# Kernel tuning notes

Hardware: AMD Instinct MI355X
Metric: run time of the kernel (lower is better)

The kernel has to match this reference:

```python
import jax, jax.numpy as jnp
import numpy as np

B, S, D = 2, 2048, 1024
H, HD = 16, 64
FFN_DIM = 4096
EPS = 1e-10


def layer_norm(x, gamma, beta):
    mean = jnp.mean(x, axis=-1, keepdims=True)
    var = jnp.mean((x - mean) ** 2, axis=-1, keepdims=True)
    return (x - mean) / jnp.sqrt(var + EPS) * gamma + beta


def setup_inputs() -> dict:
    key = jax.random.key(0)
    ks = jax.random.split(key, 12)
    s = lambda fan_in, fan_out: (6.0 / (fan_in + fan_out)) ** 0.5
    u = lambda k, shape, c: jax.random.uniform(k, shape, jnp.float32, -c, c)
    return {
        "x": jax.random.normal(ks[0], (B, S, D), jnp.float32),
        "wq": u(ks[1], (H, D, HD), s(D, HD)),
        "bq": jnp.zeros((H, HD), jnp.float32),
        "wk": u(ks[2], (H, D, HD), s(D, HD)),
        "bk": jnp.zeros((H, HD), jnp.float32),
        "wv": u(ks[3], (H, D, HD), s(D, HD)),
        "bv": jnp.zeros((H, HD), jnp.float32),
        "w_proj": u(ks[4], (D, D), s(D, D)),
        "b_proj": jnp.zeros((D,), jnp.float32),
        "gamma1": jnp.ones((D,), jnp.float32),
        "beta1": jnp.zeros((D,), jnp.float32),
        "w1": u(ks[5], (D, FFN_DIM), (1.0 / D) ** 0.5),
        "b1": jnp.zeros((FFN_DIM,), jnp.float32),
        "w2": u(ks[6], (FFN_DIM, D), (1.0 / FFN_DIM) ** 0.5),
        "b2": jnp.zeros((D,), jnp.float32),
        "gamma2": jnp.ones((D,), jnp.float32),
        "beta2": jnp.zeros((D,), jnp.float32),
    }


def reference(x, wq, bq, wk, bk, wv, bv, w_proj, b_proj, gamma1, beta1,
              w1, b1, w2, b2, gamma2, beta2):
    # multi-head self-attention (all heads batched along axis h)
    q = jnp.einsum("bsd,hde->bhse", x, wq) + bq[None, :, None, :]
    k = jnp.einsum("bsd,hde->bhse", x, wk) + bk[None, :, None, :]
    v = jnp.einsum("bsd,hde->bhse", x, wv) + bv[None, :, None, :]
    # scale by sqrt of per-head dim (emb_dim of projected queries)
    scores = jnp.einsum("bhse,bhte->bhst", q, k) / (HD ** 0.5)
    attn = jax.nn.softmax(scores, axis=-1)
    out_h = jnp.einsum("bhst,bhte->bhse", attn, v)  # [B,H,S,HD]
    concat = out_h.transpose(0, 2, 1, 3).reshape(B, S, D)
    attn_out = concat @ w_proj + b_proj
    # residual + norm1 (dropout=0)
    out1 = layer_norm(attn_out + x, gamma1, beta1)
    # FFN: linear - relu - linear
    ffn_out = jax.nn.relu(out1 @ w1 + b1) @ w2 + b2
    # residual + norm2
    return layer_norm(ffn_out + out1, gamma2, beta2)
```

## Files before the change

kernel.cpp:

```cpp
#include <hip/hip_runtime.h>
#include <stdint.h>

typedef float f32x4 __attribute__((ext_vector_type(4)));
typedef __bf16 bf16x8 __attribute__((ext_vector_type(8)));
typedef __bf16 bf16x8_a __attribute__((ext_vector_type(8), may_alias));
typedef __bf16 bf16x4_a __attribute__((ext_vector_type(4), may_alias));
typedef unsigned int u32x4_a __attribute__((ext_vector_type(4), may_alias));
typedef unsigned short u16x4_a __attribute__((ext_vector_type(4), may_alias));

#define DEV __device__ __forceinline__
#define MFMA_B16(a, b, c) __builtin_amdgcn_mfma_f32_16x16x32_bf16((a), (b), (c), 0, 0, 0)

#if __has_builtin(__builtin_amdgcn_exp2f)
#define EXP2(x) __builtin_amdgcn_exp2f(x)
#else
#define EXP2(x) exp2f(x)
#endif

DEV unsigned short f2b(float f) {
  unsigned int u = __float_as_uint(f);
  u = u + 0x7FFFu + ((u >> 16) & 1u);
  return (unsigned short)(u >> 16);
}
DEV float b2f(unsigned short u) { return __uint_as_float(((unsigned int)u) << 16); }

#define GLOAD_LDS16(gsrc, ldst)                                                  \
  __builtin_amdgcn_global_load_lds(                                              \
      (__attribute__((address_space(1))) void*)(uintptr_t)(const void*)(gsrc),   \
      (__attribute__((address_space(3))) void*)(ldst), 16, 0, 0)

__global__ __launch_bounds__(256) void prepass_kernel(
    const float* __restrict__ x, const float* __restrict__ wq,
    const float* __restrict__ wk, const float* __restrict__ wv,
    const float* __restrict__ w_proj, const float* __restrict__ w1,
    const float* __restrict__ w2, const float* __restrict__ bq,
    const float* __restrict__ bk, const float* __restrict__ bv,
    unsigned short* __restrict__ xb, unsigned short* __restrict__ Wqkv_t,
    unsigned short* __restrict__ o_proj, unsigned short* __restrict__ o1,
    unsigned short* __restrict__ o2, float* __restrict__ biasq) {
  __shared__ float tile[32][33];
  int bid = blockIdx.x;
  if (bid < 4096) {
    int i = bid * 256 + threadIdx.x;
    float4 v = ((const float4*)x)[i];
    u16x4_a t = {f2b(v.x), f2b(v.y), f2b(v.z), f2b(v.w)};
    ((u16x4_a*)xb)[i] = t;
    return;
  }
  bid -= 4096;
  if (bid < 3072) {
    const int bx = bid & 1, by = (bid >> 1) & 31, zz = bid >> 6;
    const int sel = zz >> 4, zh = zz & 15;
    const float scale = sel == 0 ? 0.18033688f : 1.f;
    const float* ip = (sel == 0 ? wq : (sel == 1 ? wk : wv)) + (size_t)zh * 1024 * 64;
    unsigned short* op = Wqkv_t + (size_t)sel * 1024 * 1024 + (size_t)zh * 1024 * 64;
    const int tx = threadIdx.x & 31, ty = threadIdx.x >> 5;
    const int c0 = bx * 32, r0 = by * 32;
#pragma unroll
    for (int j = 0; j < 32; j += 8)
      tile[ty + j][tx] = ip[(size_t)(r0 + ty + j) * 64 + (c0 + tx)];
    __syncthreads();
#pragma unroll
    for (int j = 0; j < 32; j += 8)
      op[(size_t)(c0 + ty + j) * 1024 + (r0 + tx)] = f2b(tile[tx][ty + j] * scale);
    return;
  }
  bid -= 3072;
  if (bid < 9216) {
    const float* in;
    unsigned short* out;
    int rows, cols, bx, by;
    if (bid < 1024) {
      in = w_proj; out = o_proj; rows = 1024; cols = 1024; bx = bid & 31; by = bid >> 5;
    } else if (bid < 5120) {
      bid -= 1024; in = w1; out = o1; rows = 1024; cols = 4096; bx = bid & 127; by = bid >> 7;
    } else {
      bid -= 5120; in = w2; out = o2; rows = 4096; cols = 1024; bx = bid & 31; by = bid >> 5;
    }
    const int tx = threadIdx.x & 31, ty = threadIdx.x >> 5;
    const int c0 = bx * 32, r0 = by * 32;
#pragma unroll
    for (int j = 0; j < 32; j += 8)
      tile[ty + j][tx] = in[(size_t)(r0 + ty + j) * cols + (c0 + tx)];
    __syncthreads();
#pragma unroll
    for (int j = 0; j < 32; j += 8)
      out[(size_t)(c0 + ty + j) * rows + (r0 + tx)] = f2b(tile[tx][ty + j]);
    return;
  }
  bid -= 9216;
  int c = bid * 256 + threadIdx.x;
  int which = c >> 10, idx = c & 1023;
  float v = which == 0 ? bq[idx] : (which == 1 ? bk[idx] : bv[idx]);
  biasq[c] = which == 0 ? v * 0.18033688f : v;
}

template <int EP>
__global__ __launch_bounds__(512, 2) void gemm256_kernel(
    const unsigned short* __restrict__ A, const unsigned short* __restrict__ Bt,
    int M, int N, int K, int nbx, int KS,
    const float* __restrict__ bias, unsigned short* __restrict__ outb,
    unsigned short* __restrict__ q_out, unsigned short* __restrict__ k_out,
    unsigned short* __restrict__ v_out,
    unsigned short* __restrict__ pp0, unsigned short* __restrict__ pp1,
    unsigned short* __restrict__ pp2, unsigned short* __restrict__ pp3) {
  __shared__ __align__(16) unsigned short sA[2][256 * 64];
  __shared__ __align__(16) unsigned short sB[2][256 * 64];

  const int tid = threadIdx.x;
  const int wid = tid >> 6, lane = tid & 63;
  const int g = lane >> 4, r15 = lane & 15;
  const int wm = wid >> 2, wn = wid & 3;

  const int nwg = gridDim.x, cpx = nwg >> 3, orig = blockIdx.x;
  const int wg = (orig & 7) * cpx + (orig >> 3);
  const int bx = wg % nbx;
  const int t1 = wg / nbx;
  const int kz = t1 % KS, by = t1 / KS;
  const int row0 = by * 256, col0 = bx * 256;

  const int tilesK = K >> 6;
  const int qT = tilesK / KS, rT = tilesK % KS;
  const int tile0 = kz * qT + (kz < rT ? kz : rT);
  const int NT = qT + (kz < rT ? 1 : 0);
  const int kbase = tile0 << 6;

  const unsigned short* gA0 = A + (size_t)row0 * K + kbase;
  const unsigned short* gB0 = Bt + (size_t)col0 * K + kbase;
  const int srow8 = lane >> 3;
  const int schunk = ((lane & 7) ^ srow8) * 8;

  f32x4 acc[8][4] = {};
  bf16x8 af[4][2], bfr[4][2];

  auto stA = [&](int buf, int k0, int i) {
    const int r = wid * 32 + i * 8;
    GLOAD_LDS16(gA0 + (size_t)(r + srow8) * K + k0 + schunk, &sA[buf][r * 64]);
  };
  auto stB = [&](int buf, int k0, int i) {
    const int r = wid * 32 + i * 8;
    GLOAD_LDS16(gB0 + (size_t)(r + srow8) * K + k0 + schunk, &sB[buf][r * 64]);
  };
  auto ldA = [&](const unsigned short* p, int m, int ks) -> bf16x8 {
    const int row = wm * 128 + m * 16 + r15;
    return *(const bf16x8_a*)&p[row * 64 + (((ks * 4 + g) ^ (r15 & 7)) * 8)];
  };
  auto ldB = [&](const unsigned short* p, int n, int ks) -> bf16x8 {
    const int row = wn * 64 + n * 16 + r15;
    return *(const bf16x8_a*)&p[row * 64 + (((ks * 4 + g) ^ (r15 & 7)) * 8)];
  };

#pragma unroll
  for (int i = 0; i < 4; ++i) { stA(0, 0, i); stB(0, 0, i); }
  asm volatile("s_waitcnt vmcnt(0)" ::: "memory");
  __builtin_amdgcn_s_barrier();

  for (int kt = 0; kt < NT; ++kt) {
    const int cb = kt & 1, nb = cb ^ 1;
    const bool pf = (kt + 1) < NT;
    const int k1 = (kt + 1) << 6;
    const unsigned short* pA = sA[cb];
    const unsigned short* pB = sB[cb];

#pragma unroll
    for (int m = 0; m < 4; ++m) { af[m][0] = ldA(pA, m, 0); af[m][1] = ldA(pA, m, 1); }
#pragma unroll
    for (int n = 0; n < 4; ++n) { bfr[n][0] = ldB(pB, n, 0); bfr[n][1] = ldB(pB, n, 1); }
    if (pf) { stA(nb, k1, 0); stA(nb, k1, 1); }
    __builtin_amdgcn_s_barrier();
    asm volatile("s_waitcnt lgkmcnt(0)" ::: "memory");
    __builtin_amdgcn_sched_barrier(0);
    __builtin_amdgcn_s_setprio(1);
#pragma unroll
    for (int m = 0; m < 4; ++m)
#pragma unroll
      for (int n = 0; n < 2; ++n) {
        acc[m][n] = MFMA_B16(af[m][0], bfr[n][0], acc[m][n]);
        acc[m][n] = MFMA_B16(af[m][1], bfr[n][1], acc[m][n]);
      }
    __builtin_amdgcn_s_setprio(0);
    __builtin_amdgcn_s_barrier();

    if (pf) { stA(nb, k1, 2); stA(nb, k1, 3); }
    __builtin_amdgcn_s_barrier();
    __builtin_amdgcn_s_setprio(1);
#pragma unroll
    for (int m = 0; m < 4; ++m)
#pragma unroll
      for (int n = 2; n < 4; ++n) {
        acc[m][n] = MFMA_B16(af[m][0], bfr[n][0], acc[m][n]);
        acc[m][n] = MFMA_B16(af[m][1], bfr[n][1], acc[m][n]);
      }
    __builtin_amdgcn_s_setprio(0);
    __builtin_amdgcn_s_barrier();

#pragma unroll
    for (int m = 0; m < 4; ++m) { af[m][0] = ldA(pA, m + 4, 0); af[m][1] = ldA(pA, m + 4, 1); }
    if (pf) { stB(nb, k1, 0); stB(nb, k1, 1); }
    __builtin_amdgcn_s_barrier();
    asm volatile("s_waitcnt lgkmcnt(0)" ::: "memory");
    __builtin_amdgcn_sched_barrier(0);
    __builtin_amdgcn_s_setprio(1);
#pragma unroll
    for (int m = 0; m < 4; ++m)
#pragma unroll
      for (int n = 0; n < 2; ++n) {
        acc[m + 4][n] = MFMA_B16(af[m][0], bfr[n][0], acc[m + 4][n]);
        acc[m + 4][n] = MFMA_B16(af[m][1], bfr[n][1], acc[m + 4][n]);
      }
    __builtin_amdgcn_s_setprio(0);
    __builtin_amdgcn_s_barrier();

    if (pf) { stB(nb, k1, 2); stB(nb, k1, 3); }
    __builtin_amdgcn_s_barrier();
    __builtin_amdgcn_s_setprio(1);
#pragma unroll
    for (int m = 0; m < 4; ++m)
#pragma unroll
      for (int n = 2; n < 4; ++n) {
        acc[m + 4][n] = MFMA_B16(af[m][0], bfr[n][0], acc[m + 4][n]);
        acc[m + 4][n] = MFMA_B16(af[m][1], bfr[n][1], acc[m + 4][n]);
      }
    __builtin_amdgcn_s_setprio(0);
    asm volatile("s_waitcnt vmcnt(0)" ::: "memory");
    __builtin_amdgcn_s_barrier();
  }

  unsigned short* pz = kz == 0 ? pp0 : (kz == 1 ? pp1 : (kz == 2 ? pp2 : pp3));
#pragma unroll
  for (int m = 0; m < 8; ++m) {
    const int rbase = row0 + wm * 128 + m * 16 + g * 4;
#pragma unroll
    for (int n = 0; n < 4; ++n) {
      const int col = col0 + wn * 64 + n * 16 + r15;
      const float bb = (EP == 3) ? 0.f : bias[col];
      if constexpr (EP == 0) {
        const int which = col >> 10, cc = col & 1023;
        const int hh = cc >> 6, e = cc & 63;
        const int b = rbase >> 11, s0v = rbase & 2047;
        if (which == 2) {
          bf16x4_a pk;
#pragma unroll
          for (int r = 0; r < 4; ++r) pk[r] = (__bf16)(acc[m][n][r] + bb);
          *(bf16x4_a*)(v_out + (((size_t)(b * 16 + hh) * 64) + e) * 2048 + s0v) = pk;
        } else {
          unsigned short* dst = which == 0 ? q_out : k_out;
#pragma unroll
          for (int r = 0; r < 4; ++r)
            dst[(((size_t)(b * 16 + hh) * 2048) + s0v + r) * 64 + e] =
                f2b(acc[m][n][r] + bb);
        }
      } else {
#pragma unroll
        for (int r = 0; r < 4; ++r) {
          const int row = rbase + r;
          float v = acc[m][n][r] + bb;
          if constexpr (EP == 3) {
            pz[(size_t)row * N + col] = f2b(v);
          } else {
            outb[(size_t)row * N + col] = f2b(v > 0.f ? v : 0.f);
          }
        }
      }
    }
  }
}

__global__ __launch_bounds__(256) void gemm_bt_kernel(
    const unsigned short* __restrict__ A, const unsigned short* __restrict__ Bt,
    int M, int N, int Kchunk, int Kstride,
    unsigned short* __restrict__ pp0, unsigned short* __restrict__ pp1) {
  __shared__ __align__(16) unsigned short sA[2][128 * 32];
  __shared__ __align__(16) unsigned short sB[2][128 * 32];
  const int tid = threadIdx.x;
  const int wid = tid >> 6, lane = tid & 63;
  const int g = lane >> 4, r15 = lane & 15;
  const int wr = wid >> 1, wc = wid & 1;
  const int row0 = blockIdx.y * 128, col0 = blockIdx.x * 128;
  const int kz = blockIdx.z;

  f32x4 acc[4][4] = {};

  const int c0 = wid * 128 + lane;
  const unsigned short* gA0 = A + (size_t)row0 * Kstride + (size_t)kz * Kchunk;
  const unsigned short* gB0 = Bt + (size_t)col0 * Kstride + (size_t)kz * Kchunk;

  auto stage = [&](int buf, int k0) {
#pragma unroll
    for (int j = 0; j < 2; ++j) {
      int c = c0 + j * 64;
      GLOAD_LDS16(gA0 + (size_t)(c >> 2) * Kstride + k0 + (c & 3) * 8,
                  &sA[buf][(wid * 128 + j * 64) * 8]);
      GLOAD_LDS16(gB0 + (size_t)(c >> 2) * Kstride + k0 + (c & 3) * 8,
                  &sB[buf][(wid * 128 + j * 64) * 8]);
    }
  };

  stage(0, 0);
  const int NT = Kchunk >> 5;
  for (int t = 0; t < NT; ++t) {
    const int cb = t & 1;
    __syncthreads();
    if (t + 1 < NT) stage(cb ^ 1, (t + 1) * 32);
    bf16x8 af[4], bfr[4];
#pragma unroll
    for (int m = 0; m < 4; ++m)
      af[m] = *(const bf16x8_a*)&sA[cb][(wr * 64 + m * 16 + r15) * 32 + g * 8];
#pragma unroll
    for (int n = 0; n < 4; ++n)
      bfr[n] = *(const bf16x8_a*)&sB[cb][(wc * 64 + n * 16 + r15) * 32 + g * 8];
#pragma unroll
    for (int m = 0; m < 4; ++m)
#pragma unroll
      for (int n = 0; n < 4; ++n)
        acc[m][n] = MFMA_B16(af[m], bfr[n], acc[m][n]);
  }

  unsigned short* pz = kz == 0 ? pp0 : pp1;
#pragma unroll
  for (int m = 0; m < 4; ++m) {
    const int rbase = row0 + wr * 64 + m * 16 + g * 4;
#pragma unroll
    for (int n = 0; n < 4; ++n) {
      const int col = col0 + wc * 64 + n * 16 + r15;
#pragma unroll
      for (int r = 0; r < 4; ++r)
        pz[(size_t)(rbase + r) * N + col] = f2b(acc[m][n][r]);
    }
  }
}

__global__ __launch_bounds__(256) void attn_kernel(const unsigned short* __restrict__ Q,
                                                   const unsigned short* __restrict__ K,
                                                   const unsigned short* __restrict__ Vt,
                                                   unsigned short* __restrict__ out) {
  const int flat = blockIdx.y * gridDim.x + blockIdx.x;
  const int xcd = flat & 7, rest = flat >> 3;
  const int bh = xcd * 4 + (rest >> 5);
  const int q0 = (rest & 31) * 64;

  const int tid = threadIdx.x, wid = tid >> 6, lane = tid & 63;
  const int g = lane >> 4, r15 = lane & 15;
  const int h = r15 & 7;
  const int s0 = ((g ^ h) * 8);
  const int s1 = (((g + 4) ^ h) * 8);
  const int pswz = r15 & 14;

  __shared__ __align__(16) unsigned short sK[2][64 * 64];
  __shared__ __align__(16) unsigned short sV[2][64 * 64];
  __shared__ __align__(16) unsigned short sP[4][16 * 64];

  const size_t base = (size_t)bh * (2048 * 64);
  const unsigned short* Kb = K + base;
  const unsigned short* Vb = Vt + base;

  const int qrow = q0 + wid * 16 + r15;
  bf16x8 qf[2];
  qf[0] = *(const bf16x8_a*)(Q + base + (size_t)qrow * 64 + g * 8);
  qf[1] = *(const bf16x8_a*)(Q + base + (size_t)qrow * 64 + 32 + g * 8);

  const int srow = lane >> 3;
  const int schunk = ((lane & 7) ^ srow) * 8;

  union {
    unsigned short u[8];
    bf16x8 v;
  } ou;
#pragma unroll
  for (int i = 0; i < 8; ++i) ou.u[i] = 0x3F80;
  const bf16x8 onesb = ou.v;

  f32x4 o[4] = {};
  float mrow = -1e30f, lrow = 0.f;

  const int krd0 = r15 * 64 + s0;
  const int krd1 = r15 * 64 + s1;
  unsigned short* const pw = &sP[wid][r15 * 64];
  const int pwr0 = ((2 * g) ^ pswz) << 2;
  const int pwr1 = ((8 + 2 * g) ^ pswz) << 2;

  auto stage = [&](int bufi, int kt0s) {
#pragma unroll
    for (int i = 0; i < 2; ++i) {
      const int inst = wid * 2 + i;
      const int row = 8 * inst + srow;
      GLOAD_LDS16(Kb + (size_t)(kt0s + row) * 64 + schunk, &sK[bufi][inst * 512]);
      GLOAD_LDS16(Vb + (size_t)row * 2048 + kt0s + schunk, &sV[bufi][inst * 512]);
    }
  };

  auto do_tile = [&](const unsigned short* kbuf, const unsigned short* vbuf) {
    f32x4 sc[4] = {};
#pragma unroll
    for (int kt = 0; kt < 4; ++kt) {
      bf16x8 kf0 = *(const bf16x8_a*)&kbuf[kt * 1024 + krd0];
      bf16x8 kf1 = *(const bf16x8_a*)&kbuf[kt * 1024 + krd1];
      sc[kt] = MFMA_B16(kf0, qf[0], sc[kt]);
      sc[kt] = MFMA_B16(kf1, qf[1], sc[kt]);
    }

    float a0 = fmaxf(fmaxf(sc[0][0], sc[0][1]), sc[0][2]);
    float a1 = fmaxf(fmaxf(sc[0][3], sc[1][0]), sc[1][1]);
    float a2 = fmaxf(fmaxf(sc[1][2], sc[1][3]), sc[2][0]);
    float a3 = fmaxf(fmaxf(sc[2][1], sc[2][2]), sc[2][3]);
    float a4 = fmaxf(fmaxf(sc[3][0], sc[3][1]), sc[3][2]);
    float b0 = fmaxf(fmaxf(a0, a1), a2);
    float b1 = fmaxf(fmaxf(a3, a4), sc[3][3]);
    float pmax = fmaxf(b0, b1);
    pmax = fmaxf(pmax, __shfl_xor(pmax, 16));
    pmax = fmaxf(pmax, __shfl_xor(pmax, 32));

    const bool allkeep = __all(pmax - mrow <= 11.5441f);
    float fac;
    if (allkeep) {
      fac = 1.0f;
    } else {
      float nm = fmaxf(mrow, pmax);
      fac = EXP2(mrow - nm);
      mrow = nm;
#pragma unroll
      for (int dt = 0; dt < 4; ++dt)
#pragma unroll
        for (int r = 0; r < 4; ++r) o[dt][r] *= fac;
    }

#pragma unroll
    for (int kt = 0; kt < 4; ++kt) {
      bf16x4_a pb;
      pb[0] = (__bf16)EXP2(sc[kt][0] - mrow);
      pb[1] = (__bf16)EXP2(sc[kt][1] - mrow);
      pb[2] = (__bf16)EXP2(sc[kt][2] - mrow);
      pb[3] = (__bf16)EXP2(sc[kt][3] - mrow);
      *(bf16x4_a*)&pw[((4 * kt + g) ^ pswz) << 2] = pb;
    }

    bf16x8 pf0 = *(const bf16x8_a*)&pw[pwr0];
    bf16x8 pf1 = *(const bf16x8_a*)&pw[pwr1];

    f32x4 lacc = {};
    lacc = MFMA_B16(onesb, pf0, lacc);
    lacc = MFMA_B16(onesb, pf1, lacc);
    lrow = lrow * fac + lacc[0];

#pragma unroll
    for (int dt = 0; dt < 4; ++dt) {
      bf16x8 vf0 = *(const bf16x8_a*)&vbuf[dt * 1024 + krd0];
      bf16x8 vf1 = *(const bf16x8_a*)&vbuf[dt * 1024 + krd1];
      o[dt] = MFMA_B16(vf0, pf0, o[dt]);
      o[dt] = MFMA_B16(vf1, pf1, o[dt]);
    }
  };

  stage(0, 0);
#pragma unroll 1
  for (int t = 0; t < 32; t += 2) {
    __syncthreads();
    stage(1, (t + 1) * 64);
    do_tile(&sK[0][0], &sV[0][0]);
    __syncthreads();
    if (t + 2 < 32) stage(0, (t + 2) * 64);
    do_tile(&sK[1][0], &sV[1][0]);
  }

  const int b = bh >> 4, hh = bh & 15;
  const int s = q0 + wid * 16 + r15;
  const float inv = 1.f / lrow;
  unsigned short* orow = out + ((size_t)(b * 2048 + s)) * 1024 + hh * 64;
#pragma unroll
  for (int dt = 0; dt < 4; ++dt) {
    bf16x4_a tq;
    tq[0] = (__bf16)(o[dt][0] * inv);
    tq[1] = (__bf16)(o[dt][1] * inv);
    tq[2] = (__bf16)(o[dt][2] * inv);
    tq[3] = (__bf16)(o[dt][3] * inv);
    *(bf16x4_a*)(orow + dt * 16 + g * 4) = tq;
  }
}

__global__ __launch_bounds__(256) void ln2p_kernel(
    const unsigned short* __restrict__ p0, const unsigned short* __restrict__ p1,
    const float* __restrict__ bias, const float* __restrict__ resid,
    const float* __restrict__ gamma, const float* __restrict__ beta,
    unsigned short* __restrict__ outb) {
  const int row = blockIdx.x, tid = threadIdx.x;
  const size_t off = (size_t)row * 1024;
  u16x4_a a4 = *(const u16x4_a*)(p0 + off + tid * 4);
  u16x4_a b4 = *(const u16x4_a*)(p1 + off + tid * 4);
  float4 bb4 = ((const float4*)bias)[tid];
  float4 rr = ((const float4*)(resid + off))[tid];
  float4 v;
  v.x = b2f(a4[0]) + b2f(b4[0]) + bb4.x + rr.x;
  v.y = b2f(a4[1]) + b2f(b4[1]) + bb4.y + rr.y;
  v.z = b2f(a4[2]) + b2f(b4[2]) + bb4.z + rr.z;
  v.w = b2f(a4[3]) + b2f(b4[3]) + bb4.w + rr.w;

  float s = v.x + v.y + v.z + v.w;
  float ss = v.x * v.x + v.y * v.y + v.z * v.z + v.w * v.w;
#pragma unroll
  for (int o2 = 32; o2 > 0; o2 >>= 1) {
    s += __shfl_down(s, o2);
    ss += __shfl_down(ss, o2);
  }
  __shared__ float red[8];
  const int wid = tid >> 6;
  if ((tid & 63) == 0) { red[wid] = s; red[4 + wid] = ss; }
  __syncthreads();
  float S = red[0] + red[1] + red[2] + red[3];
  float SS = red[4] + red[5] + red[6] + red[7];
  const float mean = S * (1.f / 1024.f);
  const float var = SS * (1.f / 1024.f) - mean * mean;
  const float inv = 1.f / sqrtf(var + 1e-10f);
  float4 gg = ((const float4*)gamma)[tid];
  float4 be = ((const float4*)beta)[tid];
  float4 o;
  o.x = (v.x - mean) * inv * gg.x + be.x;
  o.y = (v.y - mean) * inv * gg.y + be.y;
  o.z = (v.z - mean) * inv * gg.z + be.z;
  o.w = (v.w - mean) * inv * gg.w + be.w;
  u16x4_a t = {f2b(o.x), f2b(o.y), f2b(o.z), f2b(o.w)};
  *(u16x4_a*)(outb + off + tid * 4) = t;
}

__global__ __launch_bounds__(256) void ln4p_kernel(
    const unsigned short* __restrict__ p0, const unsigned short* __restrict__ p1,
    const unsigned short* __restrict__ p2, const unsigned short* __restrict__ p3,
    const float* __restrict__ bias, const unsigned short* __restrict__ residb,
    const float* __restrict__ gamma, const float* __restrict__ beta,
    float* __restrict__ outf) {
  const int row = blockIdx.x, tid = threadIdx.x;
  const size_t off = (size_t)row * 1024;
  u16x4_a a4 = *(const u16x4_a*)(p0 + off + tid * 4);
  u16x4_a b4 = *(const u16x4_a*)(p1 + off + tid * 4);
  u16x4_a c4 = *(const u16x4_a*)(p2 + off + tid * 4);
  u16x4_a d4 = *(const u16x4_a*)(p3 + off + tid * 4);
  u16x4_a r4 = *(const u16x4_a*)(residb + off + tid * 4);
  float4 bb4 = ((const float4*)bias)[tid];
  float4 v;
  v.x = (b2f(a4[0]) + b2f(b4[0])) + (b2f(c4[0]) + b2f(d4[0])) + bb4.x + b2f(r4[0]);
  v.y = (b2f(a4[1]) + b2f(b4[1])) + (b2f(c4[1]) + b2f(d4[1])) + bb4.y + b2f(r4[1]);
  v.z = (b2f(a4[2]) + b2f(b4[2])) + (b2f(c4[2]) + b2f(d4[2])) + bb4.z + b2f(r4[2]);
  v.w = (b2f(a4[3]) + b2f(b4[3])) + (b2f(c4[3]) + b2f(d4[3])) + bb4.w + b2f(r4[3]);

  float s = v.x + v.y + v.z + v.w;
  float ss = v.x * v.x + v.y * v.y + v.z * v.z + v.w * v.w;
#pragma unroll
  for (int o2 = 32; o2 > 0; o2 >>= 1) {
    s += __shfl_down(s, o2);
    ss += __shfl_down(ss, o2);
  }
  __shared__ float red[8];
  const int wid = tid >> 6;
  if ((tid & 63) == 0) { red[wid] = s; red[4 + wid] = ss; }
  __syncthreads();
  float S = red[0] + red[1] + red[2] + red[3];
  float SS = red[4] + red[5] + red[6] + red[7];
  const float mean = S * (1.f / 1024.f);
  const float var = SS * (1.f / 1024.f) - mean * mean;
  const float inv = 1.f / sqrtf(var + 1e-10f);
  float4 gg = ((const float4*)gamma)[tid];
  float4 be = ((const float4*)beta)[tid];
  float4 o;
  o.x = (v.x - mean) * inv * gg.x + be.x;
  o.y = (v.y - mean) * inv * gg.y + be.y;
  o.z = (v.z - mean) * inv * gg.z + be.z;
  o.w = (v.w - mean) * inv * gg.w + be.w;
  ((float4*)(outf + off))[tid] = o;
}

extern "C" void kernel_launch(void* const* d_in, const int* in_sizes, int n_in,
                              void* d_out, int out_size, void* d_ws, size_t ws_size,
                              hipStream_t stream) {
  const float* x      = (const float*)d_in[0];
  const float* wq     = (const float*)d_in[1];
  const float* bq     = (const float*)d_in[2];
  const float* wk     = (const float*)d_in[3];
  const float* bk     = (const float*)d_in[4];
  const float* wv     = (const float*)d_in[5];
  const float* bv     = (const float*)d_in[6];
  const float* w_proj = (const float*)d_in[7];
  const float* b_proj = (const float*)d_in[8];
  const float* gamma1 = (const float*)d_in[9];
  const float* beta1  = (const float*)d_in[10];
  const float* w1     = (const float*)d_in[11];
  const float* b1     = (const float*)d_in[12];
  const float* w2     = (const float*)d_in[13];
  const float* b2     = (const float*)d_in[14];
  const float* gamma2 = (const float*)d_in[15];
  const float* beta2  = (const float*)d_in[16];

  char* p = (char*)d_ws;
  auto alloc = [&](size_t bytes) {
    char* r = p;
    p += (bytes + 255) & ~(size_t)255;
    return r;
  };
  unsigned short* xb      = (unsigned short*)alloc(4096ull * 1024 * 2);
  unsigned short* Wqkv_t  = (unsigned short*)alloc(3072ull * 1024 * 2);
  unsigned short* Wproj_t = (unsigned short*)alloc(1024ull * 1024 * 2);
  unsigned short* W2t     = (unsigned short*)alloc(1024ull * 4096 * 2);
  float*          biasq   = (float*)alloc(3072 * 4);
  unsigned short* Qb      = (unsigned short*)alloc(4096ull * 1024 * 2);
  unsigned short* Kb      = (unsigned short*)alloc(4096ull * 1024 * 2);
  unsigned short* Vtb     = (unsigned short*)alloc(4096ull * 1024 * 2);
  unsigned short* W1t     = (unsigned short*)alloc(4096ull * 1024 * 2);
  unsigned short* out1b   = (unsigned short*)alloc(4096ull * 1024 * 2);
  unsigned short* ffn_h   = (unsigned short*)alloc(4096ull * 4096 * 2);
  unsigned short* concat  = xb;

  unsigned short* prA = Qb;
  unsigned short* prB = Kb;
  unsigned short* pp0 = xb;
  unsigned short* pp1 = Qb;
  unsigned short* pp2 = Kb;
  unsigned short* pp3 = Vtb;

  prepass_kernel<<<16396, 256, 0, stream>>>(x, wq, wk, wv, w_proj, w1, w2, bq, bk, bv,
                                            xb, Wqkv_t, Wproj_t, W1t, W2t, biasq);

  gemm256_kernel<0><<<192, 512, 0, stream>>>(xb, Wqkv_t, 4096, 3072, 1024, 12, 1, biasq,
                                             nullptr, Qb, Kb, Vtb, nullptr, nullptr,
                                             nullptr, nullptr);
  attn_kernel<<<dim3(32, 32), 256, 0, stream>>>(Qb, Kb, Vtb, concat);
  gemm_bt_kernel<<<dim3(8, 32, 2), 256, 0, stream>>>(concat, Wproj_t, 4096, 1024, 512, 1024,
                                                     prA, prB);
  ln2p_kernel<<<4096, 256, 0, stream>>>(prA, prB, b_proj, x, gamma1, beta1, out1b);
  gemm256_kernel<2><<<256, 512, 0, stream>>>(out1b, W1t, 4096, 4096, 1024, 16, 1, b1,
                                             ffn_h, nullptr, nullptr, nullptr,
                                             nullptr, nullptr, nullptr, nullptr);
  gemm256_kernel<3><<<256, 512, 0, stream>>>(ffn_h, W2t, 4096, 1024, 4096, 4, 4, nullptr,
                                             nullptr, nullptr, nullptr, nullptr,
                                             pp0, pp1, pp2, pp3);
  ln4p_kernel<<<4096, 256, 0, stream>>>(pp0, pp1, pp2, pp3, b2, out1b, gamma2, beta2,
                                        (float*)d_out);
}
```

Measured before the change: 234.3 us.

## Process two query tiles per attention block to reuse staged K/V tiles

Each attention workgroup now handles 128 query rows instead of 64, with every wave keeping two independent sets of Q fragments, running max/sum and output accumulators, and running both against the same staged K/V tile in shared memory. This halves K/V global loads and LDS staging per query row, and the grid shrinks to 512 blocks. In exchange, register pressure rises and fewer blocks are launched, which may lower occupancy and latency hiding on the GPU.

New measurement: 233.4 us. About the same (-0.4%).

```diff
diff --git a/kernel.cpp b/kernel.cpp
--- a/kernel.cpp
+++ b/kernel.cpp
@@ -336,8 +336,8 @@
                                                    unsigned short* __restrict__ out) {
   const int flat = blockIdx.y * gridDim.x + blockIdx.x;
   const int xcd = flat & 7, rest = flat >> 3;
-  const int bh = xcd * 4 + (rest >> 5);
-  const int q0 = (rest & 31) * 64;
+  const int bh = xcd * 4 + (rest >> 4);
+  const int q0 = (rest & 15) * 128;
 
   const int tid = threadIdx.x, wid = tid >> 6, lane = tid & 63;
   const int g = lane >> 4, r15 = lane & 15;
@@ -354,10 +354,12 @@
   const unsigned short* Kb = K + base;
   const unsigned short* Vb = Vt + base;
 
-  const int qrow = q0 + wid * 16 + r15;
-  bf16x8 qf[2];
-  qf[0] = *(const bf16x8_a*)(Q + base + (size_t)qrow * 64 + g * 8);
-  qf[1] = *(const bf16x8_a*)(Q + base + (size_t)qrow * 64 + 32 + g * 8);
+  const int qrow0 = q0 + wid * 16 + r15;
+  bf16x8 qf0[2], qf1[2];
+  qf0[0] = *(const bf16x8_a*)(Q + base + (size_t)qrow0 * 64 + g * 8);
+  qf0[1] = *(const bf16x8_a*)(Q + base + (size_t)qrow0 * 64 + 32 + g * 8);
+  qf1[0] = *(const bf16x8_a*)(Q + base + (size_t)(qrow0 + 64) * 64 + g * 8);
+  qf1[1] = *(const bf16x8_a*)(Q + base + (size_t)(qrow0 + 64) * 64 + 32 + g * 8);
 
   const int srow = lane >> 3;
   const int schunk = ((lane & 7) ^ srow) * 8;
@@ -370,8 +372,8 @@
   for (int i = 0; i < 8; ++i) ou.u[i] = 0x3F80;
   const bf16x8 onesb = ou.v;
 
-  f32x4 o[4] = {};
-  float mrow = -1e30f, lrow = 0.f;
+  f32x4 o0[4] = {}, o1[4] = {};
+  float m0 = -1e30f, l0 = 0.f, m1 = -1e30f, l1 = 0.f;
 
   const int krd0 = r15 * 64 + s0;
   const int krd1 = r15 * 64 + s1;
@@ -389,7 +391,8 @@
     }
   };
 
-  auto do_tile = [&](const unsigned short* kbuf, const unsigned short* vbuf) {
+  auto proc = [&](const unsigned short* kbuf, const unsigned short* vbuf,
+                  const bf16x8 (&qf)[2], float& mrow, float& lrow, f32x4 (&o)[4]) {
     f32x4 sc[4] = {};
 #pragma unroll
     for (int kt = 0; kt < 4; ++kt) {
@@ -451,6 +454,11 @@
     }
   };
 
+  auto do_tile = [&](const unsigned short* kbuf, const unsigned short* vbuf) {
+    proc(kbuf, vbuf, qf0, m0, l0, o0);
+    proc(kbuf, vbuf, qf1, m1, l1, o1);
+  };
+
   stage(0, 0);
 #pragma unroll 1
   for (int t = 0; t < 32; t += 2) {
@@ -464,16 +472,22 @@
 
   const int b = bh >> 4, hh = bh & 15;
   const int s = q0 + wid * 16 + r15;
-  const float inv = 1.f / lrow;
-  unsigned short* orow = out + ((size_t)(b * 2048 + s)) * 1024 + hh * 64;
+  const float inv0 = 1.f / l0, inv1 = 1.f / l1;
+  unsigned short* orow0 = out + ((size_t)(b * 2048 + s)) * 1024 + hh * 64;
+  unsigned short* orow1 = out + ((size_t)(b * 2048 + s + 64)) * 1024 + hh * 64;
 #pragma unroll
   for (int dt = 0; dt < 4; ++dt) {
-    bf16x4_a tq;
-    tq[0] = (__bf16)(o[dt][0] * inv);
-    tq[1] = (__bf16)(o[dt][1] * inv);
-    tq[2] = (__bf16)(o[dt][2] * inv);
-    tq[3] = (__bf16)(o[dt][3] * inv);
-    *(bf16x4_a*)(orow + dt * 16 + g * 4) = tq;
+    bf16x4_a t0, t1;
+    t0[0] = (__bf16)(o0[dt][0] * inv0);
+    t0[1] = (__bf16)(o0[dt][1] * inv0);
+    t0[2] = (__bf16)(o0[dt][2] * inv0);
+    t0[3] = (__bf16)(o0[dt][3] * inv0);
+    *(bf16x4_a*)(orow0 + dt * 16 + g * 4) = t0;
+    t1[0] = (__bf16)(o1[dt][0] * inv1);
+    t1[1] = (__bf16)(o1[dt][1] * inv1);
+    t1[2] = (__bf16)(o1[dt][2] * inv1);
+    t1[3] = (__bf16)(o1[dt][3] * inv1);
+    *(bf16x4_a*)(orow1 + dt * 16 + g * 4) = t1;
   }
 }
 
@@ -620,7 +634,7 @@
   gemm256_kernel<0><<<192, 512, 0, stream>>>(xb, Wqkv_t, 4096, 3072, 1024, 12, 1, biasq,
                                              nullptr, Qb, Kb, Vtb, nullptr, nullptr,
                                              nullptr, nullptr);
-  attn_kernel<<<dim3(32, 32), 256, 0, stream>>>(Qb, Kb, Vtb, concat);
+  attn_kernel<<<dim3(16, 32), 256, 0, stream>>>(Qb, Kb, Vtb, concat);
   gemm_bt_kernel<<<dim3(8, 32, 2), 256, 0, stream>>>(concat, Wproj_t, 4096, 1024, 512, 1024,
                                                      prA, prB);
   ln2p_kernel<<<4096, 256, 0, stream>>>(prA, prB, b_proj, x, gamma1, beta1, out1b);
```
